# Kernel optimization log

Measured on AMD Instinct MI355X. Metric: run time of the kernel, lower is better.

The kernel has to match this reference:

```python
import jax, jax.numpy as jnp
import numpy as np

INPUT_DIM = 1024
MEMORY_DIM = 512
MEMORY_SIZE = 4096
TOPK = 8


def setup_inputs() -> dict:
    key = jax.random.key(0)
    ks = jax.random.split(key, 7)
    query = jax.random.normal(ks[0], (8, 4096, INPUT_DIM), dtype=jnp.float32)
    memory_keys = jax.random.normal(ks[1], (MEMORY_SIZE, MEMORY_DIM), dtype=jnp.float32)
    memory_values = jax.random.normal(ks[2], (MEMORY_SIZE, MEMORY_DIM), dtype=jnp.float32)
    # nn.Linear-style init (uniform +-1/sqrt(fan_in))
    wq = jax.random.uniform(ks[3], (INPUT_DIM, MEMORY_DIM), jnp.float32, -1.0, 1.0) / np.sqrt(INPUT_DIM)
    bq = jax.random.uniform(ks[4], (MEMORY_DIM,), jnp.float32, -1.0, 1.0) / np.sqrt(INPUT_DIM)
    wo = jax.random.uniform(ks[5], (MEMORY_DIM, INPUT_DIM), jnp.float32, -1.0, 1.0) / np.sqrt(MEMORY_DIM)
    bo = jax.random.uniform(ks[6], (INPUT_DIM,), jnp.float32, -1.0, 1.0) / np.sqrt(MEMORY_DIM)
    return {"query": query, "memory_keys": memory_keys, "memory_values": memory_values,
            "wq": wq, "bq": bq, "wo": wo, "bo": bo}


def reference(query, memory_keys, memory_values, wq, bq, wo, bo):
    B, S, D = query.shape
    # Query projection: [B,S,M]
    q = jnp.einsum('bsd,dm->bsm', query, wq) + bq
    # Scores vs memory keys: [B,S,memory_size] (no expand needed)
    scores = jnp.einsum('bsm,km->bsk', q, memory_keys)
    # Top-k selection + softmax over selected scores
    topk_w, topk_idx = jax.lax.top_k(scores, TOPK)           # [B,S,K]
    topk_w = jax.nn.softmax(topk_w, axis=-1)
    # Gather selected memory values: [B,S,K,M]
    top_vals = memory_values[topk_idx]
    mem_out = jnp.einsum('bskm,bsk->bsm', top_vals, topk_w)  # weighted sum
    out = jnp.einsum('bsm,md->bsd', mem_out, wo) + bo
    return out + query
```

## Files before the change

kernel.cpp:

```cpp
#include <hip/hip_runtime.h>
#include <cstdint>

typedef _Float16 f16;
typedef uint32_t u32;
typedef f16 f16x2 __attribute__((ext_vector_type(2)));
typedef f16 f16x8 __attribute__((ext_vector_type(8)));
typedef float f32x4 __attribute__((ext_vector_type(4)));
typedef u32 u32x4 __attribute__((ext_vector_type(4)));

#define NROWS 32768
#define D_IN 1024
#define M_DIM 512
#define NKEYS 4096
#define KTOP 8

__device__ __forceinline__ u32 umax32(u32 a, u32 b) { return a > b ? a : b; }
__device__ __forceinline__ u32 umin32(u32 a, u32 b) { return a < b ? a : b; }

__device__ __forceinline__ void gload_lds16(const void* src, void* dst) {
  __builtin_amdgcn_global_load_lds(
      (const __attribute__((address_space(1))) uint32_t*)src,
      (__attribute__((address_space(3))) uint32_t*)dst, 16, 0, 0);
}

__global__ void prep_kernel(const float* __restrict__ keys, const float* __restrict__ values,
                            const float* __restrict__ wq, const float* __restrict__ wo,
                            f16* __restrict__ keys_h, f16* __restrict__ values_h,
                            f16* __restrict__ wqT, f16* __restrict__ woT) {
  const int b = blockIdx.x, t = threadIdx.x;
  if (b < 2048) {
    const float* src = (b < 1024) ? keys : values;
    f16* dst = (b < 1024) ? keys_h : values_h;
    const int bb = b & 1023;
    const size_t base = (size_t)bb * 2048 + (size_t)t * 8;
    f32x4 a = *(const f32x4*)(src + base);
    f32x4 c2 = *(const f32x4*)(src + base + 4);
    f16x8 o;
    o[0] = (f16)a[0]; o[1] = (f16)a[1]; o[2] = (f16)a[2]; o[3] = (f16)a[3];
    o[4] = (f16)c2[0]; o[5] = (f16)c2[1]; o[6] = (f16)c2[2]; o[7] = (f16)c2[3];
    *(f16x8*)(dst + base) = o;
    return;
  }
  __shared__ float lds[64][65];
  if (b < 2176) {
    const int tb = b - 2048;
    const int td = tb >> 3, tm = tb & 7;
#pragma unroll
    for (int p = 0; p < 16; ++p) {
      const int d_loc = p * 4 + (t >> 6), m_loc = t & 63;
      lds[d_loc][m_loc] = wq[(size_t)(td * 64 + d_loc) * 512 + tm * 64 + m_loc];
    }
    __syncthreads();
#pragma unroll
    for (int p = 0; p < 16; ++p) {
      const int m_loc = p * 4 + (t >> 6), d_loc = t & 63;
      wqT[(size_t)(tm * 64 + m_loc) * 1024 + td * 64 + d_loc] = (f16)lds[d_loc][m_loc];
    }
  } else {
    const int tb = b - 2176;
    const int tmm = tb >> 4, tod = tb & 15;
#pragma unroll
    for (int p = 0; p < 16; ++p) {
      const int m_loc = p * 4 + (t >> 6), od_loc = t & 63;
      lds[m_loc][od_loc] = wo[(size_t)(tmm * 64 + m_loc) * 1024 + tod * 64 + od_loc];
    }
    __syncthreads();
#pragma unroll
    for (int p = 0; p < 16; ++p) {
      const int od_loc = p * 4 + (t >> 6), m_loc = t & 63;
      woT[(size_t)(tod * 64 + od_loc) * 512 + tmm * 64 + m_loc] = (f16)lds[m_loc][od_loc];
    }
  }
}

__global__ __launch_bounds__(256, 2) void qproj_kernel(
    const float* __restrict__ query, const f16* __restrict__ wqT,
    const float* __restrict__ bq, f16* __restrict__ q_out) {
  __shared__ f16 Atile[32 * 1024];
  const int tid = threadIdx.x;
  const int wave = tid >> 6, lane = tid & 63;
  const int g = lane >> 4, c = lane & 15;
  const int rowbase = blockIdx.x * 64 + wave * 16;
  const int row = rowbase + c;

  f16x8 Breg[32];
  {
    const float* qrow = query + (size_t)row * D_IN;
#pragma unroll
    for (int kk = 0; kk < 32; ++kk) {
      f32x4 lo = *(const f32x4*)(qrow + kk * 32 + g * 8);
      f32x4 hi = *(const f32x4*)(qrow + kk * 32 + g * 8 + 4);
      f16x8 v;
      v[0] = (f16)lo[0]; v[1] = (f16)lo[1]; v[2] = (f16)lo[2]; v[3] = (f16)lo[3];
      v[4] = (f16)hi[0]; v[5] = (f16)hi[1]; v[6] = (f16)hi[2]; v[7] = (f16)hi[3];
      Breg[kk] = v;
    }
  }

  for (int mt = 0; mt < 16; ++mt) {
    __syncthreads();
#pragma unroll
    for (int i2 = 0; i2 < 8; ++i2) {
      const int kr = wave * 8 + i2;
#pragma unroll
      for (int hb = 0; hb < 2; ++hb) {
        const u32 slot = (u32)(hb * 1024 + lane * 16);
        const u32 kb = slot ^ (u32)((kr & 7) << 4);
        const char* src = (const char*)(wqT + (size_t)(mt * 32 + kr) * D_IN) + kb;
        gload_lds16(src, (char*)Atile + kr * 2048 + hb * 1024);
      }
    }
    asm volatile("s_waitcnt vmcnt(0)" ::: "memory");
    __syncthreads();

    f32x4 acc0 = {0.f, 0.f, 0.f, 0.f};
    f32x4 acc1 = {0.f, 0.f, 0.f, 0.f};
#pragma unroll
    for (int kk = 0; kk < 32; ++kk) {
      const u32 base = (u32)(kk * 64 + g * 16);
      {
        const int ml = c;
        const u32 off = (u32)(ml * 2048) + (base ^ (u32)((ml & 7) << 4));
        f16x8 a = *(const f16x8*)((const char*)Atile + off);
        acc0 = __builtin_amdgcn_mfma_f32_16x16x32_f16(a, Breg[kk], acc0, 0, 0, 0);
      }
      {
        const int ml = 16 + c;
        const u32 off = (u32)(ml * 2048) + (base ^ (u32)((ml & 7) << 4));
        f16x8 a = *(const f16x8*)((const char*)Atile + off);
        acc1 = __builtin_amdgcn_mfma_f32_16x16x32_f16(a, Breg[kk], acc1, 0, 0, 0);
      }
    }

    f32x4 bq0 = *(const f32x4*)(bq + mt * 32 + g * 4);
    f32x4 bq1 = *(const f32x4*)(bq + mt * 32 + 16 + g * 4);
    f16* qp = q_out + (size_t)row * M_DIM + mt * 32 + g * 4;
    f16x2 p;
    p[0] = (f16)(acc0[0] + bq0[0]); p[1] = (f16)(acc0[1] + bq0[1]); *(f16x2*)(qp + 0) = p;
    p[0] = (f16)(acc0[2] + bq0[2]); p[1] = (f16)(acc0[3] + bq0[3]); *(f16x2*)(qp + 2) = p;
    p[0] = (f16)(acc1[0] + bq1[0]); p[1] = (f16)(acc1[1] + bq1[1]); *(f16x2*)(qp + 16) = p;
    p[0] = (f16)(acc1[2] + bq1[2]); p[1] = (f16)(acc1[3] + bq1[3]); *(f16x2*)(qp + 18) = p;
  }
}

__global__ __launch_bounds__(512, 4) void scores_topk_kernel(
    const f16* __restrict__ q, const f16* __restrict__ keys_h,
    u32* __restrict__ cand) {
  __shared__ f16 Ktile[2][32 * 512];
  const int tid = threadIdx.x;
  const int wave = tid >> 6, lane = tid & 63;
  const int g = lane >> 4, c = lane & 15;
  const int rb = blockIdx.x >> 1, half = blockIdx.x & 1;
  const int rowbase = rb * 128 + wave * 16;
  const int myrow = rowbase + c;
  const int keybase = half * 2048;

  f16x8 Breg[16];
  {
    const f16* qr = q + (size_t)myrow * M_DIM;
#pragma unroll
    for (int kk = 0; kk < 16; ++kk)
      Breg[kk] = *(const f16x8*)(qr + kk * 32 + g * 8);
  }

  u32 topE[KTOP], topO[KTOP];
#pragma unroll
  for (int j = 0; j < KTOP; ++j) { topE[j] = 0u; topO[j] = 0u; }

  auto stage = [&](int buf, int kt) {
#pragma unroll
    for (int i2 = 0; i2 < 4; ++i2) {
      const int kr = wave * 4 + i2;
      const u32 kb = ((u32)(lane * 16)) ^ ((u32)((kr & 7) << 4));
      const char* src = (const char*)(keys_h + (size_t)(keybase + kt * 32 + kr) * M_DIM) + kb;
      gload_lds16(src, (char*)&Ktile[buf][0] + kr * 1024);
    }
  };

  stage(0, 0);
  asm volatile("s_waitcnt vmcnt(0)" ::: "memory");
  __syncthreads();

  const u32 swz = (u32)((c & 7) << 4);
  const u32 rowb0 = (u32)(c * 1024);
  const u32 rowb1 = (u32)((c + 16) * 1024);

  for (int kt = 0; kt < 64; ++kt) {
    const int cur = kt & 1;
    if (kt < 63) stage(cur ^ 1, kt + 1);

    f32x4 acc0 = {0.f, 0.f, 0.f, 0.f};
    f32x4 acc1 = {0.f, 0.f, 0.f, 0.f};
    const char* tileb = (const char*)&Ktile[cur][0];
    __builtin_amdgcn_s_setprio(1);
#pragma unroll
    for (int kk = 0; kk < 16; ++kk) {
      const u32 col = ((u32)(kk * 64 + g * 16)) ^ swz;
      f16x8 a0 = *(const f16x8*)(tileb + rowb0 + col);
      f16x8 a1 = *(const f16x8*)(tileb + rowb1 + col);
      acc0 = __builtin_amdgcn_mfma_f32_16x16x32_f16(a0, Breg[kk], acc0, 0, 0, 0);
      acc1 = __builtin_amdgcn_mfma_f32_16x16x32_f16(a1, Breg[kk], acc1, 0, 0, 0);
    }
    __builtin_amdgcn_s_setprio(0);

#pragma unroll
    for (int i = 0; i < 4; ++i) {
      {
        const float s = acc0[i];
        const u32 kidx = (u32)(keybase + kt * 32 + g * 4 + i);
        const int bi = __float_as_int(s);
        const u32 mono = (u32)bi ^ (u32)((bi >> 31) | 0x80000000);
        u32 x = ((mono + 0x800u) & 0xFFFFF000u) | kidx;
#pragma unroll
        for (int j = 0; j < KTOP; ++j) { const u32 nt = umax32(topE[j], x); x = umin32(topE[j], x); topE[j] = nt; }
      }
      {
        const float s = acc1[i];
        const u32 kidx = (u32)(keybase + kt * 32 + 16 + g * 4 + i);
        const int bi = __float_as_int(s);
        const u32 mono = (u32)bi ^ (u32)((bi >> 31) | 0x80000000);
        u32 x = ((mono + 0x800u) & 0xFFFFF000u) | kidx;
#pragma unroll
        for (int j = 0; j < KTOP; ++j) { const u32 nt = umax32(topO[j], x); x = umin32(topO[j], x); topO[j] = nt; }
      }
    }

    asm volatile("s_waitcnt vmcnt(0)" ::: "memory");
    __syncthreads();
  }

#pragma unroll
  for (int j = 0; j < KTOP; ++j) {
    u32 x = topO[j];
#pragma unroll
    for (int jj = 0; jj < KTOP; ++jj) { const u32 nt = umax32(topE[jj], x); x = umin32(topE[jj], x); topE[jj] = nt; }
  }
#pragma unroll
  for (int st = 16; st <= 32; st <<= 1) {
    u32 oth[KTOP];
#pragma unroll
    for (int j = 0; j < KTOP; ++j) oth[j] = (u32)__shfl((int)topE[j], lane ^ st);
#pragma unroll
    for (int j = 0; j < KTOP; ++j) {
      u32 x = oth[j];
#pragma unroll
      for (int jj = 0; jj < KTOP; ++jj) { const u32 nt = umax32(topE[jj], x); x = umin32(topE[jj], x); topE[jj] = nt; }
    }
  }

  if (g == 0) {
    u32* cp = cand + (size_t)myrow * 16 + half * 8;
    u32x4 a, b;
    a.x = topE[0]; a.y = topE[1]; a.z = topE[2]; a.w = topE[3];
    b.x = topE[4]; b.y = topE[5]; b.z = topE[6]; b.w = topE[7];
    *(u32x4*)(cp) = a;
    *(u32x4*)(cp + 4) = b;
  }
}

__global__ __launch_bounds__(256, 4) void merge_gather_kernel(
    const u32* __restrict__ cand, const f16* __restrict__ values_h,
    f16* __restrict__ mem_out) {
  const int tid = threadIdx.x;
  const int wave = tid >> 6, lane = tid & 63;
  const int rowbase = blockIdx.x * 32 + wave * 8;
  const int myrow = rowbase + (lane & 7);

  const u32* cp = cand + (size_t)myrow * 16;
  u32x4 a0 = *(const u32x4*)(cp);
  u32x4 a1 = *(const u32x4*)(cp + 4);
  u32x4 b0 = *(const u32x4*)(cp + 8);
  u32x4 b1 = *(const u32x4*)(cp + 12);
  u32 top[KTOP] = {a0.x, a0.y, a0.z, a0.w, a1.x, a1.y, a1.z, a1.w};
  u32 ins[KTOP] = {b0.x, b0.y, b0.z, b0.w, b1.x, b1.y, b1.z, b1.w};
#pragma unroll
  for (int j = 0; j < KTOP; ++j) {
    u32 x = ins[j];
#pragma unroll
    for (int jj = 0; jj < KTOP; ++jj) { const u32 nt = umax32(top[jj], x); x = umin32(top[jj], x); top[jj] = nt; }
  }

  float w[KTOP]; u32 idx[KTOP];
  {
    float s[KTOP];
#pragma unroll
    for (int j = 0; j < KTOP; ++j) {
      const u32 mono = top[j] & 0xFFFFF000u;
      const u32 bits = (mono & 0x80000000u) ? (mono ^ 0x80000000u) : ~mono;
      s[j] = __int_as_float(bits);
      idx[j] = top[j] & 0xFFFu;
    }
    const float m0 = s[0];
    float sum = 0.f;
#pragma unroll
    for (int j = 0; j < KTOP; ++j) { w[j] = __expf(s[j] - m0); sum += w[j]; }
    const float inv = 1.f / sum;
#pragma unroll
    for (int j = 0; j < KTOP; ++j) w[j] *= inv;
  }

  for (int r = 0; r < 8; ++r) {
    float acc2[8];
#pragma unroll
    for (int e = 0; e < 8; ++e) acc2[e] = 0.f;
#pragma unroll
    for (int j = 0; j < KTOP; ++j) {
      const u32 ix = (u32)__shfl((int)idx[j], r);
      const float wj = __shfl(w[j], r);
      const f16x8 v = *(const f16x8*)(values_h + (size_t)ix * M_DIM + lane * 8);
#pragma unroll
      for (int e = 0; e < 8; ++e) acc2[e] += wj * (float)v[e];
    }
    f16x8 o;
#pragma unroll
    for (int e = 0; e < 8; ++e) o[e] = (f16)acc2[e];
    *(f16x8*)(mem_out + (size_t)(rowbase + r) * M_DIM + lane * 8) = o;
  }
}

__global__ __launch_bounds__(256, 2) void outproj_kernel(
    const f16* __restrict__ mem_h, const f16* __restrict__ woT,
    const float* __restrict__ bo, const float* __restrict__ query,
    float* __restrict__ out) {
  __shared__ f16 Atile[32 * 512];
  const int tid = threadIdx.x;
  const int wave = tid >> 6, lane = tid & 63;
  const int g = lane >> 4, c = lane & 15;
  const int rowbase = blockIdx.x * 64 + wave * 16;
  const int row = rowbase + c;

  f16x8 Breg[16];
  {
    const f16* mr = mem_h + (size_t)row * M_DIM;
#pragma unroll
    for (int kk = 0; kk < 16; ++kk)
      Breg[kk] = *(const f16x8*)(mr + kk * 32 + g * 8);
  }

  for (int mt = 0; mt < 32; ++mt) {
    __syncthreads();
#pragma unroll
    for (int i2 = 0; i2 < 8; ++i2) {
      const int kr = wave * 8 + i2;
      const u32 kb = ((u32)(lane * 16)) ^ ((u32)((kr & 7) << 4));
      const char* src = (const char*)(woT + (size_t)(mt * 32 + kr) * M_DIM) + kb;
      gload_lds16(src, (char*)Atile + kr * 1024);
    }
    asm volatile("s_waitcnt vmcnt(0)" ::: "memory");
    __syncthreads();

    f32x4 acc0 = {0.f, 0.f, 0.f, 0.f};
    f32x4 acc1 = {0.f, 0.f, 0.f, 0.f};
#pragma unroll
    for (int kk = 0; kk < 16; ++kk) {
      const u32 base = (u32)(kk * 64 + g * 16);
      {
        const int ml = c;
        const u32 off = (u32)(ml * 1024) + (base ^ (u32)((ml & 7) << 4));
        f16x8 a = *(const f16x8*)((const char*)Atile + off);
        acc0 = __builtin_amdgcn_mfma_f32_16x16x32_f16(a, Breg[kk], acc0, 0, 0, 0);
      }
      {
        const int ml = 16 + c;
        const u32 off = (u32)(ml * 1024) + (base ^ (u32)((ml & 7) << 4));
        f16x8 a = *(const f16x8*)((const char*)Atile + off);
        acc1 = __builtin_amdgcn_mfma_f32_16x16x32_f16(a, Breg[kk], acc1, 0, 0, 0);
      }
    }

    const int od0 = mt * 32 + g * 4;
    f32x4 bo0 = *(const f32x4*)(bo + od0);
    f32x4 bo1 = *(const f32x4*)(bo + od0 + 16);
    const float* qp = query + (size_t)row * D_IN + od0;
    f32x4 q0 = *(const f32x4*)(qp);
    f32x4 q1 = *(const f32x4*)(qp + 16);
    f32x4 o0, o1;
#pragma unroll
    for (int i = 0; i < 4; ++i) {
      o0[i] = acc0[i] + bo0[i] + q0[i];
      o1[i] = acc1[i] + bo1[i] + q1[i];
    }
    float* op = out + (size_t)row * D_IN + od0;
    *(f32x4*)(op) = o0;
    *(f32x4*)(op + 16) = o1;
  }
}

extern "C" void kernel_launch(void* const* d_in, const int* in_sizes, int n_in,
                              void* d_out, int out_size, void* d_ws, size_t ws_size,
                              hipStream_t stream) {
  (void)in_sizes; (void)n_in; (void)out_size;
  const float* query = (const float*)d_in[0];
  const float* mkeys = (const float*)d_in[1];
  const float* mvals = (const float*)d_in[2];
  const float* wq    = (const float*)d_in[3];
  const float* bq    = (const float*)d_in[4];
  const float* wo    = (const float*)d_in[5];
  const float* bo    = (const float*)d_in[6];
  float* out = (float*)d_out;

  char* ws = (char*)d_ws;
  f16* keys_h   = (f16*)(ws);
  f16* values_h = (f16*)(ws + (4u << 20));
  f16* wqT      = (f16*)(ws + (8u << 20));
  f16* woT      = (f16*)(ws + (9u << 20));
  f16* q_h      = (f16*)(ws + (10u << 20));
  f16* mem_h    = (f16*)(ws + (10u << 20) + (size_t)NROWS * M_DIM * 2);
  u32* cand     = (u32*)(ws + (10u << 20) + 2ull * (size_t)NROWS * M_DIM * 2);
  const size_t need = (10u << 20) + 2ull * (size_t)NROWS * M_DIM * 2
                    + (size_t)NROWS * 16 * 4;
  if (ws_size < need) return;

  prep_kernel<<<2304, 256, 0, stream>>>(mkeys, mvals, wq, wo, keys_h, values_h, wqT, woT);
  qproj_kernel<<<NROWS / 64, 256, 0, stream>>>(query, wqT, bq, q_h);
  scores_topk_kernel<<<(NROWS / 128) * 2, 512, 0, stream>>>(q_h, keys_h, cand);
  merge_gather_kernel<<<NROWS / 32, 256, 0, stream>>>(cand, values_h, mem_h);
  outproj_kernel<<<NROWS / 64, 256, 0, stream>>>(mem_h, woT, bo, query, out);
}
```

Measured before the change: 364.8 us.

## Split key tile between LDS and direct global loads; split outproj over column halves

In the scores/top-k kernel, a quarter of each 32-key tile (rows 16-31, second half of the feature dimension) is now loaded straight from global memory into registers. Only 24 of the 32 LDS slabs are staged, using an unswizzled lane-major layout, which cuts LDS footprint and LDS traffic. The two per-thread top-8 lists are merged into one, removing the final cross-list merge at the cost of a longer serial dependency chain. The output projection launches twice as many blocks, each covering half of the output columns, with launch bounds raised to 4 waves per SIMD for more occupancy; this reloads the mem_h rows twice.

After: 496.1 us. 36.0% more time.

```diff
diff --git a/kernel.cpp b/kernel.cpp
--- a/kernel.cpp
+++ b/kernel.cpp
@@ -146,7 +146,7 @@
 __global__ __launch_bounds__(512, 4) void scores_topk_kernel(
     const f16* __restrict__ q, const f16* __restrict__ keys_h,
     u32* __restrict__ cand) {
-  __shared__ f16 Ktile[2][32 * 512];
+  __shared__ f16 Ktile[2 * 24 * 512];
   const int tid = threadIdx.x;
   const int wave = tid >> 6, lane = tid & 63;
   const int g = lane >> 4, c = lane & 15;
@@ -163,43 +163,60 @@
       Breg[kk] = *(const f16x8*)(qr + kk * 32 + g * 8);
   }
 
-  u32 topE[KTOP], topO[KTOP];
-#pragma unroll
-  for (int j = 0; j < KTOP; ++j) { topE[j] = 0u; topO[j] = 0u; }
-
+  u32 top[KTOP];
+#pragma unroll
+  for (int j = 0; j < KTOP; ++j) top[j] = 0u;
+
+  const int laneoff = c * M_DIM + g * 8;
   auto stage = [&](int buf, int kt) {
-#pragma unroll
-    for (int i2 = 0; i2 < 4; ++i2) {
-      const int kr = wave * 4 + i2;
-      const u32 kb = ((u32)(lane * 16)) ^ ((u32)((kr & 7) << 4));
-      const char* src = (const char*)(keys_h + (size_t)(keybase + kt * 32 + kr) * M_DIM) + kb;
-      gload_lds16(src, (char*)&Ktile[buf][0] + kr * 1024);
+    const f16* base = keys_h + (size_t)(keybase + kt * 32) * M_DIM + laneoff;
+    char* dbase = (char*)Ktile + buf * 24576;
+#pragma unroll
+    for (int i2 = 0; i2 < 3; ++i2) {
+      const int s = wave * 3 + i2;
+      const int srow = (s < 16) ? 0 : 16;
+      const int sdim = (s < 16) ? (s * 32) : ((s - 16) * 32);
+      gload_lds16(base + srow * M_DIM + sdim, dbase + s * 1024);
     }
   };
+
+  const f16* gp0 = keys_h + (size_t)(keybase + 16 + c) * M_DIM + g * 8;
 
   stage(0, 0);
   asm volatile("s_waitcnt vmcnt(0)" ::: "memory");
   __syncthreads();
 
-  const u32 swz = (u32)((c & 7) << 4);
-  const u32 rowb0 = (u32)(c * 1024);
-  const u32 rowb1 = (u32)((c + 16) * 1024);
+  const char* base_rd = (const char*)Ktile + lane * 16;
 
   for (int kt = 0; kt < 64; ++kt) {
     const int cur = kt & 1;
+
+    f16x8 grg[8];
+    {
+      const f16* gp = gp0 + (size_t)kt * 32 * M_DIM;
+#pragma unroll
+      for (int j = 0; j < 8; ++j)
+        grg[j] = *(const f16x8*)(gp + (8 + j) * 32);
+    }
     if (kt < 63) stage(cur ^ 1, kt + 1);
 
     f32x4 acc0 = {0.f, 0.f, 0.f, 0.f};
     f32x4 acc1 = {0.f, 0.f, 0.f, 0.f};
-    const char* tileb = (const char*)&Ktile[cur][0];
+    const char* tb = base_rd + cur * 24576;
     __builtin_amdgcn_s_setprio(1);
 #pragma unroll
     for (int kk = 0; kk < 16; ++kk) {
-      const u32 col = ((u32)(kk * 64 + g * 16)) ^ swz;
-      f16x8 a0 = *(const f16x8*)(tileb + rowb0 + col);
-      f16x8 a1 = *(const f16x8*)(tileb + rowb1 + col);
+      f16x8 a0 = *(const f16x8*)(tb + kk * 1024);
       acc0 = __builtin_amdgcn_mfma_f32_16x16x32_f16(a0, Breg[kk], acc0, 0, 0, 0);
+    }
+#pragma unroll
+    for (int kk = 0; kk < 8; ++kk) {
+      f16x8 a1 = *(const f16x8*)(tb + (16 + kk) * 1024);
       acc1 = __builtin_amdgcn_mfma_f32_16x16x32_f16(a1, Breg[kk], acc1, 0, 0, 0);
+    }
+#pragma unroll
+    for (int kk = 8; kk < 16; ++kk) {
+      acc1 = __builtin_amdgcn_mfma_f32_16x16x32_f16(grg[kk - 8], Breg[kk], acc1, 0, 0, 0);
     }
     __builtin_amdgcn_s_setprio(0);
 
@@ -212,7 +229,7 @@
         const u32 mono = (u32)bi ^ (u32)((bi >> 31) | 0x80000000);
         u32 x = ((mono + 0x800u) & 0xFFFFF000u) | kidx;
 #pragma unroll
-        for (int j = 0; j < KTOP; ++j) { const u32 nt = umax32(topE[j], x); x = umin32(topE[j], x); topE[j] = nt; }
+        for (int j = 0; j < KTOP; ++j) { const u32 nt = umax32(top[j], x); x = umin32(top[j], x); top[j] = nt; }
       }
       {
         const float s = acc1[i];
@@ -221,7 +238,7 @@
         const u32 mono = (u32)bi ^ (u32)((bi >> 31) | 0x80000000);
         u32 x = ((mono + 0x800u) & 0xFFFFF000u) | kidx;
 #pragma unroll
-        for (int j = 0; j < KTOP; ++j) { const u32 nt = umax32(topO[j], x); x = umin32(topO[j], x); topO[j] = nt; }
+        for (int j = 0; j < KTOP; ++j) { const u32 nt = umax32(top[j], x); x = umin32(top[j], x); top[j] = nt; }
       }
     }
 
@@ -229,30 +246,24 @@
     __syncthreads();
   }
 
-#pragma unroll
-  for (int j = 0; j < KTOP; ++j) {
-    u32 x = topO[j];
-#pragma unroll
-    for (int jj = 0; jj < KTOP; ++jj) { const u32 nt = umax32(topE[jj], x); x = umin32(topE[jj], x); topE[jj] = nt; }
-  }
 #pragma unroll
   for (int st = 16; st <= 32; st <<= 1) {
     u32 oth[KTOP];
 #pragma unroll
-    for (int j = 0; j < KTOP; ++j) oth[j] = (u32)__shfl((int)topE[j], lane ^ st);
+    for (int j = 0; j < KTOP; ++j) oth[j] = (u32)__shfl((int)top[j], lane ^ st);
 #pragma unroll
     for (int j = 0; j < KTOP; ++j) {
       u32 x = oth[j];
 #pragma unroll
-      for (int jj = 0; jj < KTOP; ++jj) { const u32 nt = umax32(topE[jj], x); x = umin32(topE[jj], x); topE[jj] = nt; }
+      for (int jj = 0; jj < KTOP; ++jj) { const u32 nt = umax32(top[jj], x); x = umin32(top[jj], x); top[jj] = nt; }
     }
   }
 
   if (g == 0) {
     u32* cp = cand + (size_t)myrow * 16 + half * 8;
     u32x4 a, b;
-    a.x = topE[0]; a.y = topE[1]; a.z = topE[2]; a.w = topE[3];
-    b.x = topE[4]; b.y = topE[5]; b.z = topE[6]; b.w = topE[7];
+    a.x = top[0]; a.y = top[1]; a.z = top[2]; a.w = top[3];
+    b.x = top[4]; b.y = top[5]; b.z = top[6]; b.w = top[7];
     *(u32x4*)(cp) = a;
     *(u32x4*)(cp + 4) = b;
   }
@@ -318,7 +329,7 @@
   }
 }
 
-__global__ __launch_bounds__(256, 2) void outproj_kernel(
+__global__ __launch_bounds__(256, 4) void outproj_kernel(
     const f16* __restrict__ mem_h, const f16* __restrict__ woT,
     const float* __restrict__ bo, const float* __restrict__ query,
     float* __restrict__ out) {
@@ -326,7 +337,8 @@
   const int tid = threadIdx.x;
   const int wave = tid >> 6, lane = tid & 63;
   const int g = lane >> 4, c = lane & 15;
-  const int rowbase = blockIdx.x * 64 + wave * 16;
+  const int rbk = blockIdx.x >> 1, mh = blockIdx.x & 1;
+  const int rowbase = rbk * 64 + wave * 16;
   const int row = rowbase + c;
 
   f16x8 Breg[16];
@@ -337,7 +349,7 @@
       Breg[kk] = *(const f16x8*)(mr + kk * 32 + g * 8);
   }
 
-  for (int mt = 0; mt < 32; ++mt) {
+  for (int mt = mh * 16; mt < mh * 16 + 16; ++mt) {
     __syncthreads();
 #pragma unroll
     for (int i2 = 0; i2 < 8; ++i2) {
@@ -415,5 +427,5 @@
   qproj_kernel<<<NROWS / 64, 256, 0, stream>>>(query, wqT, bq, q_h);
   scores_topk_kernel<<<(NROWS / 128) * 2, 512, 0, stream>>>(q_h, keys_h, cand);
   merge_gather_kernel<<<NROWS / 32, 256, 0, stream>>>(cand, values_h, mem_h);
-  outproj_kernel<<<NROWS / 64, 256, 0, stream>>>(mem_h, woT, bo, query, out);
-}
+  outproj_kernel<<<(NROWS / 64) * 2, 256, 0, stream>>>(mem_h, woT, bo, query, out);
+}
```

## Split qproj K across wave pairs and outproj N across two blocks for occupancy

Applied to the files above, without the earlier changes.

qproj now uses 512 threads per block, with pairs of waves each handling half of the 1024-wide reduction. This halves the register-resident query fragments so more waves fit per CU, and the partial sums are exchanged through LDS before the bias is added. outproj launches twice as many blocks, each covering half of the output columns, which raises parallelism and the occupancy target. The cost is an extra barrier and LDS exchange per qproj tile, plus duplicated mem_h row loads in outproj.

Result: faster. 348.8 us (-4.4%).

```diff
diff --git a/kernel.cpp b/kernel.cpp
--- a/kernel.cpp
+++ b/kernel.cpp
@@ -73,21 +73,23 @@
   }
 }
 
-__global__ __launch_bounds__(256, 2) void qproj_kernel(
+__global__ __launch_bounds__(512, 4) void qproj_kernel(
     const float* __restrict__ query, const f16* __restrict__ wqT,
     const float* __restrict__ bq, f16* __restrict__ q_out) {
   __shared__ f16 Atile[32 * 1024];
+  __shared__ float xchg[4 * 2 * 256];
   const int tid = threadIdx.x;
   const int wave = tid >> 6, lane = tid & 63;
   const int g = lane >> 4, c = lane & 15;
-  const int rowbase = blockIdx.x * 64 + wave * 16;
+  const int pair = wave >> 1, kp = wave & 1;
+  const int rowbase = blockIdx.x * 64 + pair * 16;
   const int row = rowbase + c;
 
-  f16x8 Breg[32];
+  f16x8 Breg[16];
   {
-    const float* qrow = query + (size_t)row * D_IN;
-#pragma unroll
-    for (int kk = 0; kk < 32; ++kk) {
+    const float* qrow = query + (size_t)row * D_IN + kp * 512;
+#pragma unroll
+    for (int kk = 0; kk < 16; ++kk) {
       f32x4 lo = *(const f32x4*)(qrow + kk * 32 + g * 8);
       f32x4 hi = *(const f32x4*)(qrow + kk * 32 + g * 8 + 4);
       f16x8 v;
@@ -97,11 +99,14 @@
     }
   }
 
+  float* xsend = xchg + pair * 512 + kp * 256 + lane * 4;
+  const float* xrecv = xchg + pair * 512 + (kp ^ 1) * 256 + lane * 4;
+
   for (int mt = 0; mt < 16; ++mt) {
     __syncthreads();
 #pragma unroll
-    for (int i2 = 0; i2 < 8; ++i2) {
-      const int kr = wave * 8 + i2;
+    for (int i2 = 0; i2 < 4; ++i2) {
+      const int kr = wave * 4 + i2;
 #pragma unroll
       for (int hb = 0; hb < 2; ++hb) {
         const u32 slot = (u32)(hb * 1024 + lane * 16);
@@ -116,8 +121,8 @@
     f32x4 acc0 = {0.f, 0.f, 0.f, 0.f};
     f32x4 acc1 = {0.f, 0.f, 0.f, 0.f};
 #pragma unroll
-    for (int kk = 0; kk < 32; ++kk) {
-      const u32 base = (u32)(kk * 64 + g * 16);
+    for (int kk = 0; kk < 16; ++kk) {
+      const u32 base = (u32)(kp * 1024 + kk * 64 + g * 16);
       {
         const int ml = c;
         const u32 off = (u32)(ml * 2048) + (base ^ (u32)((ml & 7) << 4));
@@ -132,14 +137,20 @@
       }
     }
 
-    f32x4 bq0 = *(const f32x4*)(bq + mt * 32 + g * 4);
-    f32x4 bq1 = *(const f32x4*)(bq + mt * 32 + 16 + g * 4);
-    f16* qp = q_out + (size_t)row * M_DIM + mt * 32 + g * 4;
-    f16x2 p;
-    p[0] = (f16)(acc0[0] + bq0[0]); p[1] = (f16)(acc0[1] + bq0[1]); *(f16x2*)(qp + 0) = p;
-    p[0] = (f16)(acc0[2] + bq0[2]); p[1] = (f16)(acc0[3] + bq0[3]); *(f16x2*)(qp + 2) = p;
-    p[0] = (f16)(acc1[0] + bq1[0]); p[1] = (f16)(acc1[1] + bq1[1]); *(f16x2*)(qp + 16) = p;
-    p[0] = (f16)(acc1[2] + bq1[2]); p[1] = (f16)(acc1[3] + bq1[3]); *(f16x2*)(qp + 18) = p;
+    if (kp == 0) { *(f32x4*)xsend = acc1; } else { *(f32x4*)xsend = acc0; }
+    __syncthreads();
+    {
+      f32x4 p = *(const f32x4*)xrecv;
+      f32x4 mine = (kp == 0) ? acc0 : acc1;
+      const int m0 = mt * 32 + kp * 16 + g * 4;
+      f32x4 bqv = *(const f32x4*)(bq + m0);
+      f16* qp = q_out + (size_t)row * M_DIM + m0;
+      f16x2 o;
+      o[0] = (f16)(mine[0] + p[0] + bqv[0]);
+      o[1] = (f16)(mine[1] + p[1] + bqv[1]); *(f16x2*)(qp) = o;
+      o[0] = (f16)(mine[2] + p[2] + bqv[2]);
+      o[1] = (f16)(mine[3] + p[3] + bqv[3]); *(f16x2*)(qp + 2) = o;
+    }
   }
 }
 
@@ -318,7 +329,7 @@
   }
 }
 
-__global__ __launch_bounds__(256, 2) void outproj_kernel(
+__global__ __launch_bounds__(256, 4) void outproj_kernel(
     const f16* __restrict__ mem_h, const f16* __restrict__ woT,
     const float* __restrict__ bo, const float* __restrict__ query,
     float* __restrict__ out) {
@@ -326,7 +337,8 @@
   const int tid = threadIdx.x;
   const int wave = tid >> 6, lane = tid & 63;
   const int g = lane >> 4, c = lane & 15;
-  const int rowbase = blockIdx.x * 64 + wave * 16;
+  const int rbk = blockIdx.x >> 1, mh = blockIdx.x & 1;
+  const int rowbase = rbk * 64 + wave * 16;
   const int row = rowbase + c;
 
   f16x8 Breg[16];
@@ -337,7 +349,7 @@
       Breg[kk] = *(const f16x8*)(mr + kk * 32 + g * 8);
   }
 
-  for (int mt = 0; mt < 32; ++mt) {
+  for (int mt = mh * 16; mt < mh * 16 + 16; ++mt) {
     __syncthreads();
 #pragma unroll
     for (int i2 = 0; i2 < 8; ++i2) {
@@ -412,8 +424,8 @@
   if (ws_size < need) return;
 
   prep_kernel<<<2304, 256, 0, stream>>>(mkeys, mvals, wq, wo, keys_h, values_h, wqT, woT);
-  qproj_kernel<<<NROWS / 64, 256, 0, stream>>>(query, wqT, bq, q_h);
+  qproj_kernel<<<NROWS / 64, 512, 0, stream>>>(query, wqT, bq, q_h);
   scores_topk_kernel<<<(NROWS / 128) * 2, 512, 0, stream>>>(q_h, keys_h, cand);
   merge_gather_kernel<<<NROWS / 32, 256, 0, stream>>>(cand, values_h, mem_h);
-  outproj_kernel<<<NROWS / 64, 256, 0, stream>>>(mem_h, woT, bo, query, out);
-}
+  outproj_kernel<<<(NROWS / 64) * 2, 256, 0, stream>>>(mem_h, woT, bo, query, out);
+}
```
